# Kernel tuning notes

Hardware: AMD Instinct MI355X
Metric: run time of the kernel (lower is better)

The kernel has to match this reference:

```python
import jax, jax.numpy as jnp
import numpy as np

B, D, L = 16, 256, 200
T = 1000   # max_frame_length
K = 3      # kernel_size
DW, DC = 4, 2


def setup_inputs() -> dict:
    key = jax.random.key(0)
    ks = jax.random.split(key, 16)
    plen = jax.random.randint(ks[0], (B,), 150, L + 1)
    pm = jnp.arange(L)[None, :] < plen[:, None]              # (B,L) True=valid
    phoneme_mask = pm[:, None, :]                            # (B,1,L)
    durations = jax.random.uniform(ks[1], (B, L), minval=1.0, maxval=8.0) * pm
    phoneme = jax.random.normal(ks[2], (B, D, L), dtype=jnp.float32)
    s = 0.05
    params = {
        'Wpw': jax.random.normal(ks[3], (D, D)) * s, 'bpw': jnp.zeros((D,)),
        'Cw': jax.random.normal(ks[4], (8, D, K)) * s, 'cbw': jnp.zeros((8,)),
        'Mw': jax.random.normal(ks[5], (10, DW)) * s, 'mbw': jnp.zeros((DW,)),
        'Lw': jax.random.normal(ks[6], (DW * D, D)) * s, 'lbw': jnp.zeros((D,)),
        'Wpc': jax.random.normal(ks[7], (D, D)) * s, 'bpc': jnp.zeros((D,)),
        'Cc': jax.random.normal(ks[8], (8, D, K)) * s, 'cbc': jnp.zeros((8,)),
        'Mc': jax.random.normal(ks[9], (10, DC)) * s, 'mbc': jnp.zeros((DC,)),
        'Lc': jax.random.normal(ks[10], (DW * DC, D)) * s, 'lbc': jnp.zeros((D,)),
        'Wo': jax.random.normal(ks[11], (D, 2 * D)) * s, 'bo': jnp.zeros((2 * D,)),
    }
    return {'durations': durations, 'phoneme': phoneme, 'phoneme_mask': phoneme_mask, **params}


def _conv_swish(x, W1, b1, Ck, cb, pm):
    # 1x1 conv (proj) then kernel-K 'same' conv then SiLU; mask padded phones
    h = jnp.einsum('od,bdl->bol', W1, x) + b1[None, :, None]
    h = jax.lax.conv_general_dilated(h, Ck, (1,), 'SAME',
                                     dimension_numbers=('NCH', 'OIH', 'NCH')) + cb[None, :, None]
    h = jax.nn.silu(h)
    h = jnp.where(pm[:, None, :], h, 0.0)
    return h.transpose(0, 2, 1)  # (B, L, 8)


def _mlp(S, E, h, M, mb):
    # concat start/end boundary scalars with per-phone conv features -> (B,T,L,10)
    feat = jnp.concatenate([S[..., None], E[..., None],
                            jnp.broadcast_to(h[:, None], (B, T, L, 8))], axis=-1)
    return jax.nn.silu(feat @ M + mb)


def _forward(durations, phoneme, phoneme_mask, Wpw, bpw, Cw, cbw, Mw, mbw, Lw, lbw,
             Wpc, bpc, Cc, cbc, Mc, mbc, Lc, lbc, Wo, bo):
    pm = phoneme_mask[:, 0, :]                                          # (B,L)
    frame_lengths = jnp.clip(jnp.round(durations.sum(-1)).astype(jnp.int32), 0, T)
    frame_mask = jnp.arange(T)[None, :] < frame_lengths[:, None]        # (B,T)
    attn_mask = frame_mask[:, :, None] & pm[:, None, :]                 # (B,T,L)
    sd = jnp.cumsum(durations, axis=-1)                                 # (B,L)
    sk = sd - durations
    t = jnp.arange(1, T + 1, dtype=durations.dtype)
    S = jnp.where(attn_mask, t[None, :, None] - sk[:, None, :], 0.0)    # (B,T,L)
    E = jnp.where(attn_mask, (sd - sk)[:, None, :], 0.0)                # (B,T,L)

    h_w = _conv_swish(phoneme, Wpw, bpw, Cw, cbw, pm)
    w = _mlp(S, E, h_w, Mw, mbw)                                        # (B,T,L,DW)
    w = jnp.where(pm[:, None, :, None], w, -jnp.inf)
    w = jax.nn.softmax(w, axis=2)                                       # softmax over phones
    w = jnp.where(frame_mask[:, :, None, None], w, 0.0)

    h_c = _conv_swish(phoneme, Wpc, bpc, Cc, cbc, pm)
    c = _mlp(S, E, h_c, Mc, mbc)                                        # (B,T,L,DC)

    wh = jnp.einsum('btlq,bdl->btqd', w, phoneme).reshape(B, T, DW * D) @ Lw + lbw
    wc = jnp.einsum('btlq,btlp->btqp', w, c).reshape(B, T, DW * DC) @ Lc + lbc
    whc = jnp.where(frame_mask[..., None], wh + wc, 0.0)                # (B,T,D)
    out = (whc @ Wo + bo).transpose(0, 2, 1)                            # (B,2D,T)
    return out, frame_mask, frame_lengths, w.transpose(0, 3, 1, 2)


def reference(durations, phoneme, phoneme_mask, Wpw, bpw, Cw, cbw, Mw, mbw, Lw, lbw,
              Wpc, bpc, Cc, cbc, Mc, mbc, Lc, lbc, Wo, bo):
    out, frame_mask, frame_lengths, w = _forward(
        durations, phoneme, phoneme_mask, Wpw, bpw, Cw, cbw, Mw, mbw, Lw, lbw,
        Wpc, bpc, Cc, cbc, Mc, mbc, Lc, lbc, Wo, bo)
    mean, log_std = jnp.split(out, 2, axis=1)                           # (B,D,T) each
    return (mean, log_std, frame_mask, frame_lengths, w)
```

## Files before the change

kernel.cpp:

```cpp
#include <hip/hip_runtime.h>
#include <hip/hip_bf16.h>
#include <math.h>

#define NB 16
#define ND 256
#define NL 200
#define NT 1000

typedef unsigned short ushort_t;
typedef __bf16 bf16x8 __attribute__((ext_vector_type(8)));
typedef float f32x4 __attribute__((ext_vector_type(4)));

#define OFF_FL    4981936u
#define OFF_GT    11535552u
#define OFF_WOT   15221952u
#define OFF_BASE  15287488u

__device__ __forceinline__ float silu_f(float x){ return x / (1.f + __expf(-x)); }
__device__ __forceinline__ ushort_t f2bf(float x){
  __hip_bfloat16 h = __float2bfloat16(x);
  return *(ushort_t*)&h;
}

__global__ __launch_bounds__(256, 4) void k_A(
    const float* __restrict__ dur, const float* __restrict__ ph,
    const float* __restrict__ Wp_w, const float* __restrict__ C_w, const float* __restrict__ bp_w,
    const float* __restrict__ Wp_c, const float* __restrict__ C_c, const float* __restrict__ bp_c,
    const float* __restrict__ Wo, const float* __restrict__ Lw,
    const float* __restrict__ cbw, const float* __restrict__ cbc,
    const float* __restrict__ Mw, const float* __restrict__ mbw,
    const float* __restrict__ Mc, const float* __restrict__ mbc,
    int* __restrict__ fl_ws, float* __restrict__ o_fm, float* __restrict__ o_fl,
    ushort_t* __restrict__ WoT, float4* __restrict__ base,
    ushort_t* __restrict__ Gt)
{
  __shared__ __align__(16) unsigned char smem[39936];
  int bid = blockIdx.x, tid = threadIdx.x;

  if (bid < 256){
    int b = bid >> 4, x = bid & 15;
    if (x >= 13){
      int l0 = 208 + (x - 13)*16;
      if (tid < 32)
        base[((size_t)(b*256 + l0 + (tid >> 1)))*2 + (tid & 1)] = make_float4(0,0,0,0);
      return;
    }
    float* phs  = (float*)smem;
    float* U    = (float*)(smem + 18432);
    float* ssk  = (float*)(smem + 36864);
    float (*sh)[16] = (float (*)[16])(smem + 37888);
    float* sdur = (float*)(smem + 38912);
    int l0 = x*16;

    sdur[tid & 255] = 0.f;
    __syncthreads();
    if (tid < NL) sdur[tid] = dur[b*NL + tid];
    __syncthreads();
    if (tid == 0){
      float run = 0.f;
      for (int l = 0; l < NL; ++l){ ssk[l] = run; run += sdur[l]; }
    }
    {
      const float* pr = ph + ((size_t)b*ND + tid)*NL;
      #pragma unroll
      for (int j = 0; j < 18; ++j){
        int l = l0 - 1 + j;
        phs[j*256 + tid] = (l >= 0 && l < NL) ? pr[l] : 0.f;
      }
    }
    __syncthreads();

    for (int br = 0; br < 2; ++br){
      const float* Wp  = br ? Wp_c : Wp_w;
      const float* bpv = br ? bp_c : bp_w;
      {
        int i = tid;
        float u[18];
        float bb = bpv[i];
        #pragma unroll
        for (int j = 0; j < 18; ++j) u[j] = bb;
        const float4* wr = (const float4*)(Wp + (size_t)i*ND);
        for (int d4 = 0; d4 < 64; ++d4){
          float4 a = wr[d4];
          #pragma unroll
          for (int j = 0; j < 18; ++j){
            float4 p = *(const float4*)&phs[j*256 + d4*4];
            u[j] += a.x*p.x + a.y*p.y + a.z*p.z + a.w*p.w;
          }
        }
        #pragma unroll
        for (int j = 0; j < 18; ++j){
          int l = l0 - 1 + j;
          bool pad = (l < 0 || l >= NL);
          U[i*18 + j] = pad ? 0.f : u[j];
        }
      }
      __syncthreads();
      if (tid < 128){
        int lu = tid >> 3, oc = tid & 7;
        int l = l0 + lu;
        float h = 0.f;
        if (l < NL){
          const float* C = br ? C_c : C_w;
          float val = (br ? cbc : cbw)[oc];
          #pragma unroll 4
          for (int i = 0; i < ND; ++i){
            const float* cc = C + ((size_t)oc*ND + i)*3;
            val += cc[0]*U[i*18 + lu] + cc[1]*U[i*18 + lu + 1] + cc[2]*U[i*18 + lu + 2];
          }
          float pm = (sdur[l] > 0.5f) ? 1.f : 0.f;
          h = silu_f(val) * pm;
        }
        sh[lu][br*8 + oc] = h;
      }
      __syncthreads();
    }
    if (tid < 16){
      int ll = x*16 + tid;
      float4 o0 = make_float4(0,0,0,0);
      float4 o1 = make_float4(0,0,0,0);
      if (ll < NL){
        float dl  = sdur[ll];
        float pm  = (dl > 0.5f) ? 1.f : 0.f;
        float skl = ssk[ll];
        float c1[4], c2[2];
        #pragma unroll
        for (int q = 0; q < 4; ++q) c1[q] = mbw[q] + dl*Mw[4 + q] - skl*Mw[q];
        #pragma unroll
        for (int p = 0; p < 2; ++p) c2[p] = mbc[p] + dl*Mc[2 + p] - skl*Mc[p];
        #pragma unroll
        for (int j = 0; j < 8; ++j){
          float hwv = sh[tid][j], hcv = sh[tid][8 + j];
          #pragma unroll
          for (int q = 0; q < 4; ++q) c1[q] += hwv*Mw[(2 + j)*4 + q];
          #pragma unroll
          for (int p = 0; p < 2; ++p) c2[p] += hcv*Mc[(2 + j)*2 + p];
        }
        o0 = make_float4(c1[0], c1[1], c1[2], c1[3]);
        o1 = make_float4(c2[0], c2[1], pm, 0.f);
      }
      base[((size_t)(b*256 + ll))*2 + 0] = o0;
      base[((size_t)(b*256 + ll))*2 + 1] = o1;
    }
  } else if (bid < 512){
    int r = bid - 256;
    int xb = r & 1, yb = (r >> 1) & 1, bq = r >> 2;
    int b = bq >> 2, q = bq & 3;
    int m0 = yb * 128;
    int n0 = xb * 128;
    int lane = tid & 63, wave = tid >> 6;
    int wm = wave >> 1, wn = wave & 1;
    int col = lane & 15, kg4 = lane >> 4;
    ushort_t (*Asub)[72] = (ushort_t (*)[72])smem;
    ushort_t (*Bsub)[72] = (ushort_t (*)[72])(smem + 18432);
    int na = lane*2;

    f32x4 acc[4][4] = {};
    for (int kq = 0; kq < 4; ++kq){
      int d0 = kq*64;
      for (int rep = 0; rep < 16; ++rep){
        int dk = wave*16 + rep;
        float2 v = *(const float2*)(Lw + ((size_t)(q*256 + d0 + dk))*ND + m0 + na);
        Asub[na    ][dk] = f2bf(v.x);
        Asub[na + 1][dk] = f2bf(v.y);
      }
      for (int rep = 0; rep < 16; ++rep){
        int dk = wave*16 + rep;
        int l = n0 + na;
        float2 v; v.x = 0.f; v.y = 0.f;
        if (l < NL)
          v = *(const float2*)(ph + ((size_t)b*ND + d0 + dk)*NL + l);
        Bsub[na    ][dk] = f2bf(v.x);
        Bsub[na + 1][dk] = f2bf(v.y);
      }
      __syncthreads();
      for (int kt = 0; kt < 2; ++kt){
        int k0 = kt*32;
        bf16x8 afr[4], bfr[4];
        #pragma unroll
        for (int i = 0; i < 4; ++i)
          afr[i] = *(const bf16x8*)&Asub[wm*64 + i*16 + col][k0 + kg4*8];
        #pragma unroll
        for (int j = 0; j < 4; ++j)
          bfr[j] = *(const bf16x8*)&Bsub[wn*64 + j*16 + col][k0 + kg4*8];
        #pragma unroll
        for (int i = 0; i < 4; ++i)
          #pragma unroll
          for (int j = 0; j < 4; ++j)
            acc[i][j] = __builtin_amdgcn_mfma_f32_16x16x32_bf16(afr[i], bfr[j], acc[i][j], 0, 0, 0);
      }
      __syncthreads();
    }
    ushort_t (*st2)[136] = (ushort_t (*)[136])smem;
    int rq = lane >> 4;
    #pragma unroll
    for (int i = 0; i < 4; ++i){
      #pragma unroll
      for (int rr = 0; rr < 4; ++rr){
        int rl = wm*64 + i*16 + rq*4 + rr;
        #pragma unroll
        for (int j = 0; j < 4; ++j){
          int cl = wn*64 + j*16 + col;
          st2[rl][cl] = f2bf(acc[i][j][rr]);
        }
      }
    }
    __syncthreads();
    #pragma unroll
    for (int rep = 0; rep < 8; ++rep){
      int row = rep*16 + (tid >> 4);
      int ch  = tid & 15;
      int l   = n0 + ch*8;
      if (l < NL){
        int n = m0 + row;
        *(uint4*)(Gt + ((size_t)(b*ND + n))*800 + q*NL + l) = *(const uint4*)&st2[row][ch*8];
      }
    }
  } else if (bid < 528){
    int b = bid - 512;
    float* sdur = (float*)smem;
    int* sfl = (int*)(sdur + 256);
    if (tid < NL) sdur[tid] = dur[b*NL + tid];
    __syncthreads();
    if (tid == 0){
      float run = 0.f;
      for (int l = 0; l < NL; ++l) run += sdur[l];
      int fl = (int)rintf(run);
      fl = fl < 0 ? 0 : (fl > NT ? NT : fl);
      sfl[0] = fl; fl_ws[b] = fl; o_fl[b] = (float)fl;
    }
    __syncthreads();
    int flv = sfl[0];
    for (int t = tid; t < NT; t += 256) o_fm[b*NT + t] = (t < flv) ? 1.f : 0.f;
  } else {
    int base_id = (bid - 528)*256 + tid;
    #pragma unroll
    for (int rep = 0; rep < 4; ++rep){
      int gid = rep*32768 + base_id;
      int n = gid >> 8, k = gid & 255;
      WoT[gid] = f2bf(Wo[(size_t)k*512 + n]);
    }
  }
}

#define AP 808
#define TT 64
__global__ __launch_bounds__(1024, 4) void k_wv_fused(
    const float4* __restrict__ base,
    const int* __restrict__ fl_ws,
    const float* __restrict__ Mw, const float* __restrict__ Mc,
    const ushort_t* __restrict__ Gt,
    const float* __restrict__ Lc,
    const float* __restrict__ lbc,
    const float* __restrict__ lbw,
    const ushort_t* __restrict__ WoT,
    const float* __restrict__ bo,
    float* __restrict__ wout,
    float* __restrict__ o_mean, float* __restrict__ o_lstd)
{
  __shared__ ushort_t As[TT*AP];
  __shared__ float    wcs[TT][8];
  int b = blockIdx.x;
  int m0 = blockIdx.y * TT;
  int tid = threadIdx.x, lane = tid & 63, wave = tid >> 6;
  int col = lane & 15, kg4 = lane >> 4;
  int fl = fl_ws[b];

  if (fl <= m0){
    for (int idx = tid; idx < TT*4*50; idx += 1024){
      int tl = idx / 200;
      int rqs = idx - tl*200;
      int q = rqs / 50, seg = rqs - q*50;
      int t = m0 + tl;
      if (t < NT)
        *(float4*)&wout[(((size_t)(b*4 + q))*NT + t)*NL + seg*4] = make_float4(0,0,0,0);
    }
    for (int idx = tid; idx < 512*16; idx += 1024){
      int s = idx >> 4, j = idx & 15;
      int t0 = m0 + j*4;
      if (t0 + 3 < NT){
        float v = bo[s];
        float4 v4 = make_float4(v, v, v, v);
        if (s < ND) *(float4*)&o_mean[((size_t)b*ND + s)*NT + t0] = v4;
        else        *(float4*)&o_lstd[((size_t)b*ND + (s - ND))*NT + t0] = v4;
      }
    }
    return;
  }

  int l0 = lane*4;
  bool lv = (l0 < NL);

  #pragma unroll
  for (int s = 0; s < 4; ++s){
    int tl = wave*4 + s, t = m0 + tl;
    if (t < fl) continue;
    for (int k = l0; k < 800; k += 256){
      uint2 zz2; zz2.x = 0u; zz2.y = 0u;
      *(uint2*)&As[tl*AP + k] = zz2;
    }
    if (lane < 8) wcs[tl][lane] = 0.f;
    if (t < NT && lv){
      float4 z4 = make_float4(0,0,0,0);
      #pragma unroll
      for (int q = 0; q < 4; ++q)
        *(float4*)&wout[(((size_t)(b*4 + q))*NT + t)*NL + l0] = z4;
    }
  }

  float b0a[4][4], b1x[4], b1y[4], pmv[4];
  #pragma unroll
  for (int e = 0; e < 4; ++e){
    float4 v0 = make_float4(0,0,0,0), v1 = make_float4(0,0,0,0);
    if (lv){
      v0 = base[((size_t)(b*256 + l0 + e))*2 + 0];
      v1 = base[((size_t)(b*256 + l0 + e))*2 + 1];
    }
    b0a[e][0] = v0.x; b0a[e][1] = v0.y; b0a[e][2] = v0.z; b0a[e][3] = v0.w;
    b1x[e] = v1.x; b1y[e] = v1.y; pmv[e] = v1.z;
  }
  float mwq[4] = {Mw[0], Mw[1], Mw[2], Mw[3]};
  float mcp[2] = {Mc[0], Mc[1]};

  for (int sp = 0; sp < 2; ++sp){
    int tl0 = wave*4 + sp*2;
    int t0 = m0 + tl0;
    if (t0 >= fl) break;
    bool a1 = (t0 + 1 < fl);
    float tf[2] = {(float)(t0 + 1), (float)(t0 + 2)};

    float z[2][4][4], mx[2][4];
    #pragma unroll
    for (int u = 0; u < 2; ++u)
      #pragma unroll
      for (int q = 0; q < 4; ++q) mx[u][q] = -INFINITY;
    #pragma unroll
    for (int e = 0; e < 4; ++e){
      #pragma unroll
      for (int u = 0; u < 2; ++u){
        #pragma unroll
        for (int q = 0; q < 4; ++q){
          float sv = silu_f(b0a[e][q] + tf[u]*mwq[q]);
          float zv = (pmv[e] > 0.f) ? sv : -INFINITY;
          z[u][e][q] = zv;
          mx[u][q] = fmaxf(mx[u][q], zv);
        }
      }
    }
    #pragma unroll
    for (int u = 0; u < 2; ++u)
      #pragma unroll
      for (int q = 0; q < 4; ++q){
        float v = mx[u][q];
        #pragma unroll
        for (int off = 32; off; off >>= 1) v = fmaxf(v, __shfl_xor(v, off));
        mx[u][q] = v;
      }
    float is4[2][4] = {{0,0,0,0},{0,0,0,0}};
    #pragma unroll
    for (int e = 0; e < 4; ++e){
      #pragma unroll
      for (int u = 0; u < 2; ++u){
        #pragma unroll
        for (int q = 0; q < 4; ++q){
          float ev = (pmv[e] > 0.f) ? __expf(z[u][e][q] - mx[u][q]) : 0.f;
          z[u][e][q] = ev;
          is4[u][q] += ev;
        }
      }
    }
    #pragma unroll
    for (int u = 0; u < 2; ++u)
      #pragma unroll
      for (int q = 0; q < 4; ++q){
        float v = is4[u][q];
        #pragma unroll
        for (int off = 32; off; off >>= 1) v += __shfl_xor(v, off);
        is4[u][q] = 1.f / v;
      }
    float cv[2][4][2];
    #pragma unroll
    for (int e = 0; e < 4; ++e)
      #pragma unroll
      for (int u = 0; u < 2; ++u){
        cv[u][e][0] = silu_f(b1x[e] + tf[u]*mcp[0]);
        cv[u][e][1] = silu_f(b1y[e] + tf[u]*mcp[1]);
      }
    float wc[2][8];
    #pragma unroll
    for (int u = 0; u < 2; ++u)
      #pragma unroll
      for (int x = 0; x < 8; ++x) wc[u][x] = 0.f;
    #pragma unroll
    for (int u = 0; u < 2; ++u){
      bool act = (u == 0) || a1;
      int t = t0 + u, tl = tl0 + u;
      #pragma unroll
      for (int q = 0; q < 4; ++q){
        float w0 = z[u][0][q]*is4[u][q];
        float w1 = z[u][1][q]*is4[u][q];
        float w2 = z[u][2][q]*is4[u][q];
        float w3 = z[u][3][q]*is4[u][q];
        if (act && lv){
          *(float4*)&wout[(((size_t)(b*4 + q))*NT + t)*NL + l0] =
              make_float4(w0, w1, w2, w3);
          uint2 pk;
          pk.x = (unsigned)f2bf(w0) | ((unsigned)f2bf(w1) << 16);
          pk.y = (unsigned)f2bf(w2) | ((unsigned)f2bf(w3) << 16);
          *(uint2*)&As[tl*AP + q*NL + l0] = pk;
        }
        wc[u][q*2 + 0] += w0*cv[u][0][0] + w1*cv[u][1][0] + w2*cv[u][2][0] + w3*cv[u][3][0];
        wc[u][q*2 + 1] += w0*cv[u][0][1] + w1*cv[u][1][1] + w2*cv[u][2][1] + w3*cv[u][3][1];
      }
    }
    #pragma unroll
    for (int u = 0; u < 2; ++u){
      if (u == 1 && !a1) break;
      #pragma unroll
      for (int x = 0; x < 8; ++x){
        float v = wc[u][x];
        #pragma unroll
        for (int off = 32; off; off >>= 1) v += __shfl_xor(v, off);
        wc[u][x] = v;
      }
      if (lane == 0){
        #pragma unroll
        for (int x = 0; x < 8; ++x) wcs[tl0 + u][x] = wc[u][x];
      }
    }
  }
  __syncthreads();

  f32x4 acc[4] = {};
  const ushort_t* Gb = Gt + (size_t)b*ND*800;
  for (int kt = 0; kt < 25; ++kt){
    int k0 = kt*32;
    bf16x8 afr[4], bfr;
    #pragma unroll
    for (int i = 0; i < 4; ++i)
      afr[i] = *(const bf16x8*)(&As[(i*16 + col)*AP + k0 + kg4*8]);
    bfr = *(const bf16x8*)(Gb + ((size_t)(wave*16 + col))*800 + k0 + kg4*8);
    #pragma unroll
    for (int i = 0; i < 4; ++i)
      acc[i] = __builtin_amdgcn_mfma_f32_16x16x32_bf16(afr[i], bfr, acc[i], 0, 0, 0);
  }
  __syncthreads();

  ushort_t (*stc)[264] = (ushort_t (*)[264])As;
  {
    int rq = lane >> 4;
    int n = wave*16 + col;
    float lbn = lbc[n], lbwn = lbw[n];
    float lcn[8];
    #pragma unroll
    for (int u = 0; u < 8; ++u) lcn[u] = Lc[u*ND + n];
    #pragma unroll
    for (int i = 0; i < 4; ++i){
      #pragma unroll
      for (int r = 0; r < 4; ++r){
        int tl = i*16 + rq*4 + r;
        int t = m0 + tl;
        if (t < NT){
          float f = (t < fl) ? 1.f : 0.f;
          float vcv = lbn
            + wcs[tl][0]*lcn[0] + wcs[tl][1]*lcn[1]
            + wcs[tl][2]*lcn[2] + wcs[tl][3]*lcn[3]
            + wcs[tl][4]*lcn[4] + wcs[tl][5]*lcn[5]
            + wcs[tl][6]*lcn[6] + wcs[tl][7]*lcn[7];
          stc[tl][n] = f2bf(f * (acc[i][r] + lbwn + vcv));
        }
      }
    }
  }
  __syncthreads();

  {
    f32x4 acc2[2][4] = {};
    for (int kt = 0; kt < 8; ++kt){
      int k0 = kt*32;
      bf16x8 afr[2], bfr[4];
      #pragma unroll
      for (int j = 0; j < 4; ++j)
        bfr[j] = *(const bf16x8*)(&stc[j*16 + col][k0 + kg4*8]);
      #pragma unroll
      for (int i = 0; i < 2; ++i)
        afr[i] = *(const bf16x8*)(WoT + ((size_t)(wave*32 + i*16 + col))*ND + k0 + kg4*8);
      #pragma unroll
      for (int i = 0; i < 2; ++i)
        #pragma unroll
        for (int j = 0; j < 4; ++j)
          acc2[i][j] = __builtin_amdgcn_mfma_f32_16x16x32_bf16(afr[i], bfr[j], acc2[i][j], 0, 0, 0);
    }
    int rq = lane >> 4;
    #pragma unroll
    for (int i = 0; i < 2; ++i){
      #pragma unroll
      for (int r = 0; r < 4; ++r){
        int s = wave*32 + i*16 + rq*4 + r;
        float bov = bo[s];
        #pragma unroll
        for (int j = 0; j < 4; ++j){
          int t = m0 + j*16 + col;
          if (t < NT){
            float v = acc2[i][j][r] + bov;
            if (s < ND) o_mean[((size_t)b*ND + s)*NT + t] = v;
            else        o_lstd[((size_t)b*ND + (s - ND))*NT + t] = v;
          }
        }
      }
    }
  }
}

extern "C" void kernel_launch(void* const* d_in, const int* in_sizes, int n_in,
                              void* d_out, int out_size, void* d_ws, size_t ws_size,
                              hipStream_t stream)
{
  const float* dur = (const float*)d_in[0];
  const float* ph  = (const float*)d_in[1];
  const float* Wpw = (const float*)d_in[3];
  const float* bpw = (const float*)d_in[4];
  const float* Cw  = (const float*)d_in[5];
  const float* cbw = (const float*)d_in[6];
  const float* Mw  = (const float*)d_in[7];
  const float* mbw = (const float*)d_in[8];
  const float* Lw  = (const float*)d_in[9];
  const float* lbw = (const float*)d_in[10];
  const float* Wpc = (const float*)d_in[11];
  const float* bpc = (const float*)d_in[12];
  const float* Cc  = (const float*)d_in[13];
  const float* cbc = (const float*)d_in[14];
  const float* Mc  = (const float*)d_in[15];
  const float* mbc = (const float*)d_in[16];
  const float* Lc  = (const float*)d_in[17];
  const float* lbc = (const float*)d_in[18];
  const float* Wo  = (const float*)d_in[19];
  const float* bo  = (const float*)d_in[20];

  float* out    = (float*)d_out;
  float* o_mean = out;
  float* o_lstd = out + (size_t)NB*ND*NT;
  float* o_fm   = o_lstd + (size_t)NB*ND*NT;
  float* o_fl   = o_fm + NB*NT;
  float* o_w    = o_fl + NB;

  float* ws   = (float*)d_ws;
  int*   fl   = (int*)(ws + OFF_FL);
  ushort_t* Gt   = (ushort_t*)(ws + OFF_GT);
  ushort_t* WoT  = (ushort_t*)(ws + OFF_WOT);
  float4*   base = (float4*)(ws + OFF_BASE);

  k_A<<<656, 256, 0, stream>>>(dur, ph, Wpw, Cw, bpw, Wpc, Cc, bpc, Wo, Lw,
                               cbw, cbc, Mw, mbw, Mc, mbc,
                               fl, o_fm, o_fl, WoT, base, Gt);
  {
    dim3 g(NB, 16);
    k_wv_fused<<<g, 1024, 0, stream>>>(base, fl, Mw, Mc, Gt, Lc, lbc, lbw,
                                       WoT, bo, o_w, o_mean, o_lstd);
  }
}
```

Before: 256.5 us.

## Fold 1x1 projection into kernel-3 conv weights via precomputed combined matrix

Precomputes the composed weights E = C·Wp (and the projected bias) in a small new stage-1 kernel, so per-phone conv features become a direct dot product of phoneme columns with 24 combined rows per branch. This replaces the per-tile 256x256 projection matmul over 18 phone columns followed by the 256-deep conv reduction. The frame-length/mask work moves into the stage-1 kernel, which adds one extra launch and a dependency between kernels.

```diff
diff --git a/kernel.cpp b/kernel.cpp
--- a/kernel.cpp
+++ b/kernel.cpp
@@ -11,6 +11,10 @@
 typedef __bf16 bf16x8 __attribute__((ext_vector_type(8)));
 typedef float f32x4 __attribute__((ext_vector_type(4)));
 
+#define OFF_EW    4969600u
+#define OFF_EC    4975744u
+#define OFF_BW2   4981888u
+#define OFF_BC2   4981912u
 #define OFF_FL    4981936u
 #define OFF_GT    11535552u
 #define OFF_WOT   15221952u
@@ -22,19 +26,64 @@
   return *(ushort_t*)&h;
 }
 
-__global__ __launch_bounds__(256, 4) void k_A(
-    const float* __restrict__ dur, const float* __restrict__ ph,
+__global__ __launch_bounds__(256) void k_stage1(
+    const float* __restrict__ dur,
     const float* __restrict__ Wp_w, const float* __restrict__ C_w, const float* __restrict__ bp_w,
     const float* __restrict__ Wp_c, const float* __restrict__ C_c, const float* __restrict__ bp_c,
-    const float* __restrict__ Wo, const float* __restrict__ Lw,
+    int* __restrict__ fl_ws, float* __restrict__ o_fm, float* __restrict__ o_fl,
+    float* __restrict__ Ew, float* __restrict__ Ec,
+    float* __restrict__ bw2, float* __restrict__ bc2)
+{
+  int bid = blockIdx.x, tid = threadIdx.x;
+  if (bid < 16){
+    int b = bid;
+    __shared__ float sdur[NL];
+    __shared__ int sfl;
+    if (tid < NL) sdur[tid] = dur[b*NL + tid];
+    __syncthreads();
+    if (tid == 0){
+      float run = 0.f;
+      for (int l = 0; l < NL; ++l) run += sdur[l];
+      int fl = (int)rintf(run);
+      fl = fl < 0 ? 0 : (fl > NT ? NT : fl);
+      sfl = fl; fl_ws[b] = fl; o_fl[b] = (float)fl;
+    }
+    __syncthreads();
+    for (int t = tid; t < NT; t += 256) o_fm[b*NT + t] = (t < sfl) ? 1.f : 0.f;
+  } else {
+    int sbid = bid - 16;
+    int gid = sbid*256 + tid;
+    int branch = gid / 6144;
+    int r = gid % 6144;
+    int d = r & 255;
+    int ock = r >> 8;
+    int oc = ock / 3, k = ock % 3;
+    const float* Wp = branch ? Wp_c : Wp_w;
+    const float* C  = branch ? C_c  : C_w;
+    float acc = 0.f;
+    for (int i = 0; i < ND; ++i) acc += C[(oc*ND + i)*3 + k] * Wp[i*ND + d];
+    (branch ? Ec : Ew)[r] = acc;
+    if (d == 0){
+      const float* bp = branch ? bp_c : bp_w;
+      float bb = 0.f;
+      for (int i = 0; i < ND; ++i) bb += C[(oc*ND + i)*3 + k] * bp[i];
+      (branch ? bc2 : bw2)[ock] = bb;
+    }
+  }
+}
+
+__global__ __launch_bounds__(256, 4) void k_stage2(
+    const float* __restrict__ dur, const float* __restrict__ ph,
+    const float* __restrict__ Ew, const float* __restrict__ Ec,
+    const float* __restrict__ bw2, const float* __restrict__ bc2,
     const float* __restrict__ cbw, const float* __restrict__ cbc,
     const float* __restrict__ Mw, const float* __restrict__ mbw,
     const float* __restrict__ Mc, const float* __restrict__ mbc,
-    int* __restrict__ fl_ws, float* __restrict__ o_fm, float* __restrict__ o_fl,
-    ushort_t* __restrict__ WoT, float4* __restrict__ base,
-    ushort_t* __restrict__ Gt)
+    const float* __restrict__ Lw, const float* __restrict__ Wo,
+    float4* __restrict__ base, ushort_t* __restrict__ Gt,
+    ushort_t* __restrict__ WoT)
 {
-  __shared__ __align__(16) unsigned char smem[39936];
+  __shared__ __align__(16) unsigned char smem[36864];
   int bid = blockIdx.x, tid = threadIdx.x;
 
   if (bid < 256){
@@ -46,14 +95,11 @@
       return;
     }
     float* phs  = (float*)smem;
-    float* U    = (float*)(smem + 18432);
-    float* ssk  = (float*)(smem + 36864);
-    float (*sh)[16] = (float (*)[16])(smem + 37888);
-    float* sdur = (float*)(smem + 38912);
+    float* sdur = (float*)(smem + 18432);
+    float* ssk  = (float*)(smem + 19456);
+    float (*sh)[17] = (float (*)[17])(smem + 20480);
     int l0 = x*16;
 
-    sdur[tid & 255] = 0.f;
-    __syncthreads();
     if (tid < NL) sdur[tid] = dur[b*NL + tid];
     __syncthreads();
     if (tid == 0){
@@ -69,52 +115,35 @@
       }
     }
     __syncthreads();
-
-    for (int br = 0; br < 2; ++br){
-      const float* Wp  = br ? Wp_c : Wp_w;
-      const float* bpv = br ? bp_c : bp_w;
-      {
-        int i = tid;
-        float u[18];
-        float bb = bpv[i];
-        #pragma unroll
-        for (int j = 0; j < 18; ++j) u[j] = bb;
-        const float4* wr = (const float4*)(Wp + (size_t)i*ND);
-        for (int d4 = 0; d4 < 64; ++d4){
-          float4 a = wr[d4];
-          #pragma unroll
-          for (int j = 0; j < 18; ++j){
-            float4 p = *(const float4*)&phs[j*256 + d4*4];
-            u[j] += a.x*p.x + a.y*p.y + a.z*p.z + a.w*p.w;
+    {
+      int lu = tid >> 4, u = tid & 15;
+      int l = l0 + lu;
+      float h = 0.f;
+      if (l < NL){
+        int branch = u >> 3, oc = u & 7;
+        const float* E  = branch ? Ec  : Ew;
+        const float* b2 = branch ? bc2 : bw2;
+        float val = (branch ? cbc : cbw)[oc];
+        #pragma unroll
+        for (int k = 0; k < 3; ++k){
+          int ll = l + k - 1;
+          if (ll < 0 || ll >= NL) continue;
+          float acc = b2[oc*3 + k];
+          const float4* Er = (const float4*)(E + (oc*3 + k)*ND);
+          const float4* pr = (const float4*)&phs[(lu + k)*256];
+          #pragma unroll 8
+          for (int d = 0; d < 64; ++d){
+            float4 e = Er[d], p = pr[d];
+            acc += e.x*p.x + e.y*p.y + e.z*p.z + e.w*p.w;
           }
-        }
-        #pragma unroll
-        for (int j = 0; j < 18; ++j){
-          int l = l0 - 1 + j;
-          bool pad = (l < 0 || l >= NL);
-          U[i*18 + j] = pad ? 0.f : u[j];
-        }
-      }
-      __syncthreads();
-      if (tid < 128){
-        int lu = tid >> 3, oc = tid & 7;
-        int l = l0 + lu;
-        float h = 0.f;
-        if (l < NL){
-          const float* C = br ? C_c : C_w;
-          float val = (br ? cbc : cbw)[oc];
-          #pragma unroll 4
-          for (int i = 0; i < ND; ++i){
-            const float* cc = C + ((size_t)oc*ND + i)*3;
-            val += cc[0]*U[i*18 + lu] + cc[1]*U[i*18 + lu + 1] + cc[2]*U[i*18 + lu + 2];
-          }
-          float pm = (sdur[l] > 0.5f) ? 1.f : 0.f;
-          h = silu_f(val) * pm;
-        }
-        sh[lu][br*8 + oc] = h;
-      }
-      __syncthreads();
-    }
+          val += acc;
+        }
+        float pm = (sdur[l] > 0.5f) ? 1.f : 0.f;
+        h = silu_f(val) * pm;
+      }
+      sh[lu][u] = h;
+    }
+    __syncthreads();
     if (tid < 16){
       int ll = x*16 + tid;
       float4 o0 = make_float4(0,0,0,0);
@@ -216,24 +245,8 @@
         *(uint4*)(Gt + ((size_t)(b*ND + n))*800 + q*NL + l) = *(const uint4*)&st2[row][ch*8];
       }
     }
-  } else if (bid < 528){
-    int b = bid - 512;
-    float* sdur = (float*)smem;
-    int* sfl = (int*)(sdur + 256);
-    if (tid < NL) sdur[tid] = dur[b*NL + tid];
-    __syncthreads();
-    if (tid == 0){
-      float run = 0.f;
-      for (int l = 0; l < NL; ++l) run += sdur[l];
-      int fl = (int)rintf(run);
-      fl = fl < 0 ? 0 : (fl > NT ? NT : fl);
-      sfl[0] = fl; fl_ws[b] = fl; o_fl[b] = (float)fl;
-    }
-    __syncthreads();
-    int flv = sfl[0];
-    for (int t = tid; t < NT; t += 256) o_fm[b*NT + t] = (t < flv) ? 1.f : 0.f;
   } else {
-    int base_id = (bid - 528)*256 + tid;
+    int base_id = (bid - 512)*256 + tid;
     #pragma unroll
     for (int rep = 0; rep < 4; ++rep){
       int gid = rep*32768 + base_id;
@@ -545,14 +558,19 @@
   float* o_w    = o_fl + NB;
 
   float* ws   = (float*)d_ws;
+  float* Ew   = ws + OFF_EW;
+  float* Ec   = ws + OFF_EC;
+  float* bw2  = ws + OFF_BW2;
+  float* bc2  = ws + OFF_BC2;
   int*   fl   = (int*)(ws + OFF_FL);
   ushort_t* Gt   = (ushort_t*)(ws + OFF_GT);
   ushort_t* WoT  = (ushort_t*)(ws + OFF_WOT);
   float4*   base = (float4*)(ws + OFF_BASE);
 
-  k_A<<<656, 256, 0, stream>>>(dur, ph, Wpw, Cw, bpw, Wpc, Cc, bpc, Wo, Lw,
-                               cbw, cbc, Mw, mbw, Mc, mbc,
-                               fl, o_fm, o_fl, WoT, base, Gt);
+  k_stage1<<<64, 256, 0, stream>>>(dur, Wpw, Cw, bpw, Wpc, Cc, bpc,
+                                   fl, o_fm, o_fl, Ew, Ec, bw2, bc2);
+  k_stage2<<<640, 256, 0, stream>>>(dur, ph, Ew, Ec, bw2, bc2, cbw, cbc,
+                                    Mw, mbw, Mc, mbc, Lw, Wo, base, Gt, WoT);
   {
     dim3 g(NB, 16);
     k_wv_fused<<<g, 1024, 0, stream>>>(base, fl, Mw, Mc, Gt, Lc, lbc, lbw,
```

New measurement: 226.2 us. -11.8%, faster.

## Split projection across branches and move kernel-3 conv into fused frame kernel

Applied to the files above, without the earlier changes.

The pre-kernel now gives each (batch, tile, branch) its own block for the 1x1 projection, writing U transposed to workspace instead of doing both branches and the conv serially in one block. The kernel-3 conv, SiLU and per-phone MLP base terms are recomputed inside each active k_wv_fused block from U and a transposed conv weight copy, so they land in shared memory. This doubles parallelism in the first kernel and shortens its critical path. In exchange, every frame tile block redundantly recomputes the conv for all phones of its batch.

```diff
diff --git a/kernel.cpp b/kernel.cpp
--- a/kernel.cpp
+++ b/kernel.cpp
@@ -11,10 +11,12 @@
 typedef __bf16 bf16x8 __attribute__((ext_vector_type(8)));
 typedef float f32x4 __attribute__((ext_vector_type(4)));
 
+#define OFF_UT    0u
+#define OFF_CT    4000000u
+#define OFF_SK    4966400u
 #define OFF_FL    4981936u
 #define OFF_GT    11535552u
 #define OFF_WOT   15221952u
-#define OFF_BASE  15287488u
 
 __device__ __forceinline__ float silu_f(float x){ return x / (1.f + __expf(-x)); }
 __device__ __forceinline__ ushort_t f2bf(float x){
@@ -22,44 +24,44 @@
   return *(ushort_t*)&h;
 }
 
-__global__ __launch_bounds__(256, 4) void k_A(
+__global__ __launch_bounds__(256) void k_pre(
     const float* __restrict__ dur, const float* __restrict__ ph,
     const float* __restrict__ Wp_w, const float* __restrict__ C_w, const float* __restrict__ bp_w,
     const float* __restrict__ Wp_c, const float* __restrict__ C_c, const float* __restrict__ bp_c,
     const float* __restrict__ Wo, const float* __restrict__ Lw,
-    const float* __restrict__ cbw, const float* __restrict__ cbc,
-    const float* __restrict__ Mw, const float* __restrict__ mbw,
-    const float* __restrict__ Mc, const float* __restrict__ mbc,
-    int* __restrict__ fl_ws, float* __restrict__ o_fm, float* __restrict__ o_fl,
-    ushort_t* __restrict__ WoT, float4* __restrict__ base,
-    ushort_t* __restrict__ Gt)
+    float* __restrict__ sk_ws, int* __restrict__ fl_ws,
+    float* __restrict__ o_fm, float* __restrict__ o_fl,
+    float* __restrict__ U_T, float* __restrict__ Ct,
+    ushort_t* __restrict__ WoT, ushort_t* __restrict__ Gt)
 {
-  __shared__ __align__(16) unsigned char smem[39936];
+  __shared__ __align__(16) unsigned char smem[36864];
   int bid = blockIdx.x, tid = threadIdx.x;
 
-  if (bid < 256){
-    int b = bid >> 4, x = bid & 15;
-    if (x >= 13){
-      int l0 = 208 + (x - 13)*16;
-      if (tid < 32)
-        base[((size_t)(b*256 + l0 + (tid >> 1)))*2 + (tid & 1)] = make_float4(0,0,0,0);
-      return;
-    }
-    float* phs  = (float*)smem;
-    float* U    = (float*)(smem + 18432);
-    float* ssk  = (float*)(smem + 36864);
-    float (*sh)[16] = (float (*)[16])(smem + 37888);
-    float* sdur = (float*)(smem + 38912);
-    int l0 = x*16;
-
-    sdur[tid & 255] = 0.f;
-    __syncthreads();
+  if (bid < 16){
+    int b = bid;
+    float* sdur = (float*)smem;
+    float* ssk  = sdur + 256;
+    int*   sfl  = (int*)(ssk + 256);
     if (tid < NL) sdur[tid] = dur[b*NL + tid];
     __syncthreads();
     if (tid == 0){
       float run = 0.f;
       for (int l = 0; l < NL; ++l){ ssk[l] = run; run += sdur[l]; }
-    }
+      int fl = (int)rintf(run);
+      fl = fl < 0 ? 0 : (fl > NT ? NT : fl);
+      sfl[0] = fl; fl_ws[b] = fl; o_fl[b] = (float)fl;
+    }
+    __syncthreads();
+    if (tid < NL) sk_ws[b*NL + tid] = ssk[tid];
+    int flv = sfl[0];
+    for (int t = tid; t < NT; t += 256) o_fm[b*NT + t] = (t < flv) ? 1.f : 0.f;
+  } else if (bid < 432){
+    int r = bid - 16;
+    int br = r & 1;
+    int bx = r >> 1;
+    int x = bx % 13, b = bx / 13;
+    int l0 = x*16;
+    float* phs = (float*)smem;
     {
       const float* pr = ph + ((size_t)b*ND + tid)*NL;
       #pragma unroll
@@ -69,81 +71,28 @@
       }
     }
     __syncthreads();
-
-    for (int br = 0; br < 2; ++br){
-      const float* Wp  = br ? Wp_c : Wp_w;
-      const float* bpv = br ? bp_c : bp_w;
-      {
-        int i = tid;
-        float u[18];
-        float bb = bpv[i];
-        #pragma unroll
-        for (int j = 0; j < 18; ++j) u[j] = bb;
-        const float4* wr = (const float4*)(Wp + (size_t)i*ND);
-        for (int d4 = 0; d4 < 64; ++d4){
-          float4 a = wr[d4];
-          #pragma unroll
-          for (int j = 0; j < 18; ++j){
-            float4 p = *(const float4*)&phs[j*256 + d4*4];
-            u[j] += a.x*p.x + a.y*p.y + a.z*p.z + a.w*p.w;
-          }
-        }
-        #pragma unroll
-        for (int j = 0; j < 18; ++j){
-          int l = l0 - 1 + j;
-          bool pad = (l < 0 || l >= NL);
-          U[i*18 + j] = pad ? 0.f : u[j];
-        }
-      }
-      __syncthreads();
-      if (tid < 128){
-        int lu = tid >> 3, oc = tid & 7;
-        int l = l0 + lu;
-        float h = 0.f;
-        if (l < NL){
-          const float* C = br ? C_c : C_w;
-          float val = (br ? cbc : cbw)[oc];
-          #pragma unroll 4
-          for (int i = 0; i < ND; ++i){
-            const float* cc = C + ((size_t)oc*ND + i)*3;
-            val += cc[0]*U[i*18 + lu] + cc[1]*U[i*18 + lu + 1] + cc[2]*U[i*18 + lu + 2];
-          }
-          float pm = (sdur[l] > 0.5f) ? 1.f : 0.f;
-          h = silu_f(val) * pm;
-        }
-        sh[lu][br*8 + oc] = h;
-      }
-      __syncthreads();
-    }
-    if (tid < 16){
-      int ll = x*16 + tid;
-      float4 o0 = make_float4(0,0,0,0);
-      float4 o1 = make_float4(0,0,0,0);
-      if (ll < NL){
-        float dl  = sdur[ll];
-        float pm  = (dl > 0.5f) ? 1.f : 0.f;
-        float skl = ssk[ll];
-        float c1[4], c2[2];
-        #pragma unroll
-        for (int q = 0; q < 4; ++q) c1[q] = mbw[q] + dl*Mw[4 + q] - skl*Mw[q];
-        #pragma unroll
-        for (int p = 0; p < 2; ++p) c2[p] = mbc[p] + dl*Mc[2 + p] - skl*Mc[p];
-        #pragma unroll
-        for (int j = 0; j < 8; ++j){
-          float hwv = sh[tid][j], hcv = sh[tid][8 + j];
-          #pragma unroll
-          for (int q = 0; q < 4; ++q) c1[q] += hwv*Mw[(2 + j)*4 + q];
-          #pragma unroll
-          for (int p = 0; p < 2; ++p) c2[p] += hcv*Mc[(2 + j)*2 + p];
-        }
-        o0 = make_float4(c1[0], c1[1], c1[2], c1[3]);
-        o1 = make_float4(c2[0], c2[1], pm, 0.f);
-      }
-      base[((size_t)(b*256 + ll))*2 + 0] = o0;
-      base[((size_t)(b*256 + ll))*2 + 1] = o1;
-    }
-  } else if (bid < 512){
-    int r = bid - 256;
+    int i = tid;
+    float u[18];
+    float bb = (br ? bp_c : bp_w)[i];
+    #pragma unroll
+    for (int j = 0; j < 18; ++j) u[j] = bb;
+    const float4* wr = (const float4*)((br ? Wp_c : Wp_w) + (size_t)i*ND);
+    for (int d4 = 0; d4 < 64; ++d4){
+      float4 a = wr[d4];
+      #pragma unroll
+      for (int j = 0; j < 18; ++j){
+        float4 p = *(const float4*)&phs[j*256 + d4*4];
+        u[j] += a.x*p.x + a.y*p.y + a.z*p.z + a.w*p.w;
+      }
+    }
+    float* Ub = U_T + ((size_t)(br*16 + b))*NL*ND;
+    #pragma unroll
+    for (int j = 1; j <= 16; ++j){
+      int l = l0 - 1 + j;
+      if (l < NL) Ub[(size_t)l*ND + i] = u[j];
+    }
+  } else if (bid < 688){
+    int r = bid - 432;
     int xb = r & 1, yb = (r >> 1) & 1, bq = r >> 2;
     int b = bq >> 2, q = bq & 3;
     int m0 = yb * 128;
@@ -216,37 +165,32 @@
         *(uint4*)(Gt + ((size_t)(b*ND + n))*800 + q*NL + l) = *(const uint4*)&st2[row][ch*8];
       }
     }
-  } else if (bid < 528){
-    int b = bid - 512;
-    float* sdur = (float*)smem;
-    int* sfl = (int*)(sdur + 256);
-    if (tid < NL) sdur[tid] = dur[b*NL + tid];
-    __syncthreads();
-    if (tid == 0){
-      float run = 0.f;
-      for (int l = 0; l < NL; ++l) run += sdur[l];
-      int fl = (int)rintf(run);
-      fl = fl < 0 ? 0 : (fl > NT ? NT : fl);
-      sfl[0] = fl; fl_ws[b] = fl; o_fl[b] = (float)fl;
-    }
-    __syncthreads();
-    int flv = sfl[0];
-    for (int t = tid; t < NT; t += 256) o_fm[b*NT + t] = (t < flv) ? 1.f : 0.f;
-  } else {
-    int base_id = (bid - 528)*256 + tid;
+  } else if (bid < 816){
+    int base_id = (bid - 688)*256 + tid;
     #pragma unroll
     for (int rep = 0; rep < 4; ++rep){
       int gid = rep*32768 + base_id;
       int n = gid >> 8, k = gid & 255;
       WoT[gid] = f2bf(Wo[(size_t)k*512 + n]);
     }
+  } else {
+    for (int idx = tid; idx < 12288; idx += 256){
+      int br = idx / 6144, r = idx % 6144;
+      int oc = r / 768, k = (r % 768) / 256, i = r & 255;
+      Ct[idx] = (br ? C_c : C_w)[((size_t)oc*ND + i)*3 + k];
+    }
   }
 }
 
 #define AP 808
 #define TT 64
 __global__ __launch_bounds__(1024, 4) void k_wv_fused(
-    const float4* __restrict__ base,
+    const float* __restrict__ U_T,
+    const float* __restrict__ Ct,
+    const float* __restrict__ dur,
+    const float* __restrict__ sk_ws,
+    const float* __restrict__ cbw, const float* __restrict__ cbc,
+    const float* __restrict__ mbw, const float* __restrict__ mbc,
     const int* __restrict__ fl_ws,
     const float* __restrict__ Mw, const float* __restrict__ Mc,
     const ushort_t* __restrict__ Gt,
@@ -260,6 +204,7 @@
 {
   __shared__ ushort_t As[TT*AP];
   __shared__ float    wcs[TT][8];
+  __shared__ float    baseL[NL][9];
   int b = blockIdx.x;
   int m0 = blockIdx.y * TT;
   int tid = threadIdx.x, lane = tid & 63, wave = tid >> 6;
@@ -288,6 +233,58 @@
     return;
   }
 
+  {
+    float* hL = (float*)As;
+    for (int idx = tid; idx < NL*16; idx += 1024){
+      int l = idx >> 4, u = idx & 15;
+      int br = u >> 3, oc = u & 7;
+      const float* Cb = Ct + ((size_t)(br*8 + oc))*3*256;
+      const float* Ub = U_T + ((size_t)(br*16 + b))*NL*ND;
+      float val = (br ? cbc : cbw)[oc];
+      #pragma unroll
+      for (int k = 0; k < 3; ++k){
+        int ll = l + k - 1;
+        if (ll < 0 || ll >= NL) continue;
+        const float4* cr = (const float4*)(Cb + k*256);
+        const float4* ur = (const float4*)(Ub + (size_t)ll*ND);
+        float acc = 0.f;
+        #pragma unroll 8
+        for (int d = 0; d < 64; ++d){
+          float4 c4 = cr[d], u4 = ur[d];
+          acc += c4.x*u4.x + c4.y*u4.y + c4.z*u4.z + c4.w*u4.w;
+        }
+        val += acc;
+      }
+      float pm = (dur[b*NL + l] > 0.5f) ? 1.f : 0.f;
+      hL[l*16 + u] = silu_f(val) * pm;
+    }
+    __syncthreads();
+    if (tid < NL){
+      int l = tid;
+      float dl  = dur[b*NL + l];
+      float pm  = (dl > 0.5f) ? 1.f : 0.f;
+      float skl = sk_ws[b*NL + l];
+      float c1[4], c2[2];
+      #pragma unroll
+      for (int q = 0; q < 4; ++q) c1[q] = mbw[q] + dl*Mw[4 + q] - skl*Mw[q];
+      #pragma unroll
+      for (int p = 0; p < 2; ++p) c2[p] = mbc[p] + dl*Mc[2 + p] - skl*Mc[p];
+      #pragma unroll
+      for (int j = 0; j < 8; ++j){
+        float hwv = hL[l*16 + j], hcv = hL[l*16 + 8 + j];
+        #pragma unroll
+        for (int q = 0; q < 4; ++q) c1[q] += hwv*Mw[(2 + j)*4 + q];
+        #pragma unroll
+        for (int p = 0; p < 2; ++p) c2[p] += hcv*Mc[(2 + j)*2 + p];
+      }
+      baseL[l][0] = c1[0]; baseL[l][1] = c1[1];
+      baseL[l][2] = c1[2]; baseL[l][3] = c1[3];
+      baseL[l][4] = c2[0]; baseL[l][5] = c2[1];
+      baseL[l][6] = pm;    baseL[l][7] = 0.f;
+    }
+    __syncthreads();
+  }
+
   int l0 = lane*4;
   bool lv = (l0 < NL);
 
@@ -311,13 +308,14 @@
   float b0a[4][4], b1x[4], b1y[4], pmv[4];
   #pragma unroll
   for (int e = 0; e < 4; ++e){
-    float4 v0 = make_float4(0,0,0,0), v1 = make_float4(0,0,0,0);
     if (lv){
-      v0 = base[((size_t)(b*256 + l0 + e))*2 + 0];
-      v1 = base[((size_t)(b*256 + l0 + e))*2 + 1];
-    }
-    b0a[e][0] = v0.x; b0a[e][1] = v0.y; b0a[e][2] = v0.z; b0a[e][3] = v0.w;
-    b1x[e] = v1.x; b1y[e] = v1.y; pmv[e] = v1.z;
+      const float* bl = &baseL[l0 + e][0];
+      b0a[e][0] = bl[0]; b0a[e][1] = bl[1]; b0a[e][2] = bl[2]; b0a[e][3] = bl[3];
+      b1x[e] = bl[4]; b1y[e] = bl[5]; pmv[e] = bl[6];
+    } else {
+      b0a[e][0] = b0a[e][1] = b0a[e][2] = b0a[e][3] = 0.f;
+      b1x[e] = 0.f; b1y[e] = 0.f; pmv[e] = 0.f;
+    }
   }
   float mwq[4] = {Mw[0], Mw[1], Mw[2], Mw[3]};
   float mcp[2] = {Mc[0], Mc[1]};
@@ -545,17 +543,19 @@
   float* o_w    = o_fl + NB;
 
   float* ws   = (float*)d_ws;
+  float* U_T  = ws + OFF_UT;
+  float* Ct   = ws + OFF_CT;
+  float* sk   = ws + OFF_SK;
   int*   fl   = (int*)(ws + OFF_FL);
   ushort_t* Gt   = (ushort_t*)(ws + OFF_GT);
   ushort_t* WoT  = (ushort_t*)(ws + OFF_WOT);
-  float4*   base = (float4*)(ws + OFF_BASE);
-
-  k_A<<<656, 256, 0, stream>>>(dur, ph, Wpw, Cw, bpw, Wpc, Cc, bpc, Wo, Lw,
-                               cbw, cbc, Mw, mbw, Mc, mbc,
-                               fl, o_fm, o_fl, WoT, base, Gt);
+
+  k_pre<<<817, 256, 0, stream>>>(dur, ph, Wpw, Cw, bpw, Wpc, Cc, bpc, Wo, Lw,
+                                 sk, fl, o_fm, o_fl, U_T, Ct, WoT, Gt);
   {
     dim3 g(NB, 16);
-    k_wv_fused<<<g, 1024, 0, stream>>>(base, fl, Mw, Mc, Gt, Lc, lbc, lbw,
+    k_wv_fused<<<g, 1024, 0, stream>>>(U_T, Ct, dur, sk, cbw, cbc, mbw, mbc,
+                                       fl, Mw, Mc, Gt, Lc, lbc, lbw,
                                        WoT, bo, o_w, o_mean, o_lstd);
   }
 }
```

After: 539.8 us. 2.1x slower.
